# Kernel optimization log

Hardware: AMD Instinct MI355X
Metric: run time of the kernel (lower is better)

Reference implementation:

```python
import jax, jax.numpy as jnp
import numpy as np

NEG_SLOPE = 0.2

def edge_softmax(logits, dst, num_nodes):
    # logits: [E, H]; softmax over incoming edges of each dst node, per head
    m = jax.ops.segment_max(logits, dst, num_segments=num_nodes)  # [N, H]
    e = jnp.exp(logits - m[dst])
    s = jax.ops.segment_sum(e, dst, num_segments=num_nodes)  # [N, H]
    return e / s[dst]

def gat_layer(h, src, dst, W, al, ar, b, activation):
    # W: [F_in, H*D], al/ar: [H, D], b: [H, D]
    N = h.shape[0]
    H, D = al.shape
    feat = (h @ W).reshape(N, H, D)
    el = jnp.sum(feat * al, axis=-1)  # [N, H]
    er = jnp.sum(feat * ar, axis=-1)  # [N, H]
    e = jax.nn.leaky_relu(el[src] + er[dst], NEG_SLOPE)  # [E, H]
    a = edge_softmax(e, dst, N)  # [E, H]
    msg = feat[src] * a[:, :, None]  # [E, H, D]
    rst = jax.ops.segment_sum(msg, dst, num_segments=N) + b[None]  # [N, H, D]
    if activation:
        rst = jax.nn.relu(rst)
    return rst

def setup_inputs() -> dict:
    key = jax.random.key(0)
    ks = jax.random.split(key, 16)
    N, E = 50000, 800000
    IN, HID, OUT, H = 128, 64, 64, 4
    s = 0.1
    return {
        "features": jax.random.normal(ks[0], (N, IN), jnp.float32),
        "src": jax.random.randint(ks[1], (E,), 0, N),
        "dst": jax.random.randint(ks[2], (E,), 0, N),
        "W1": jax.random.normal(ks[3], (IN, H * HID), jnp.float32) * s,
        "al1": jax.random.normal(ks[4], (H, HID), jnp.float32) * s,
        "ar1": jax.random.normal(ks[5], (H, HID), jnp.float32) * s,
        "b1": jnp.zeros((H, HID), jnp.float32),
        "W2": jax.random.normal(ks[6], (H * HID, H * HID), jnp.float32) * s,
        "al2": jax.random.normal(ks[7], (H, HID), jnp.float32) * s,
        "ar2": jax.random.normal(ks[8], (H, HID), jnp.float32) * s,
        "b2": jnp.zeros((H, HID), jnp.float32),
        "W3": jax.random.normal(ks[9], (H * HID, OUT), jnp.float32) * s,
        "al3": jax.random.normal(ks[10], (1, OUT), jnp.float32) * s,
        "ar3": jax.random.normal(ks[11], (1, OUT), jnp.float32) * s,
        "b3": jnp.zeros((1, OUT), jnp.float32),
    }

def reference(features, src, dst, W1, al1, ar1, b1, W2, al2, ar2, b2, W3, al3, ar3, b3):
    N = features.shape[0]
    h = gat_layer(features, src, dst, W1, al1, ar1, b1, activation=True)   # [N, 4, 64]
    h = h.reshape(N, -1)                                                    # [N, 256]
    h = gat_layer(h, src, dst, W2, al2, ar2, b2, activation=True)          # [N, 4, 64]
    h = h.reshape(N, -1)                                                    # [N, 256]
    h = gat_layer(h, src, dst, W3, al3, ar3, b3, activation=False)         # [N, 1, 64]
    return h.mean(axis=1)                                                   # [N, 64]
```

## Files before the change

kernel.cpp:

```cpp
#include <hip/hip_runtime.h>
#include <hip/hip_bf16.h>

#define LEAKY 0.2f
#define LOG2E 1.44269504f

typedef __attribute__((ext_vector_type(8))) short short8;
typedef __attribute__((ext_vector_type(4))) float f32x4;

__device__ inline unsigned short f2b(float f) {
    unsigned u = __float_as_uint(f);
    u += 0x7FFFu + ((u >> 16) & 1u);
    return (unsigned short)(u >> 16);
}
__device__ inline float b2f(unsigned short s) {
    return __uint_as_float(((unsigned)s) << 16);
}
__device__ inline float fexp2(float x) { return __builtin_amdgcn_exp2f(x); }

#define NEB 8192



__global__ __launch_bounds__(256)
void k_prep(const float* __restrict__ features, unsigned short* __restrict__ fconv,
            int n4,
            const float* __restrict__ W1, const float* __restrict__ W2,
            const float* __restrict__ W3, unsigned short* __restrict__ Wt1,
            unsigned short* __restrict__ Wt2, unsigned short* __restrict__ Wt3,
            const int* __restrict__ dst, int* __restrict__ hist, int nbb,
            int E, int N) {
    __shared__ int lc[256];
    const int tid = threadIdx.x;
    if (blockIdx.x < nbb) {
        lc[tid] = 0;
        __syncthreads();
        const int b0 = blockIdx.x * NEB;
        const int cnt = min(NEB, E - b0);
        for (int j = 0; j < NEB / 256; ++j) {
            int idx = j * 256 + tid;
            if (idx < cnt) {
                int dn = dst[b0 + idx];
                if ((unsigned)dn < (unsigned)N) atomicAdd(&lc[dn >> 8], 1);
            }
        }
        __syncthreads();
        hist[blockIdx.x * 256 + tid] = lc[tid];
        return;
    }
    int idx = (blockIdx.x - nbb) * 256 + tid;
    if (idx < n4) {
        float4 v = *(const float4*)(features + idx * 4);
        ushort4 o;
        o.x = f2b(v.x); o.y = f2b(v.y); o.z = f2b(v.z); o.w = f2b(v.w);
        *(ushort4*)(fconv + idx * 4) = o;
        return;
    }
    int j = idx - n4;
    if (j < 32768) {
        int m = j >> 7, k = j & 127;
        Wt1[j] = f2b(W1[(size_t)k * 256 + m]);
        return;
    }
    if (j < 98304) {
        int jj = j - 32768;
        int m = jj >> 8, ks = jj & 255;
        int kt = (ks & 192) | ((ks & 3) << 4) | ((ks & 63) >> 2);
        Wt2[jj] = f2b(W2[(size_t)kt * 256 + m]);
        return;
    }
    if (j < 114688) {
        int jj = j - 98304;
        int m = jj >> 8, ks = jj & 255;
        int kt = (ks & 192) | ((ks & 3) << 4) | ((ks & 63) >> 2);
        Wt3[jj] = f2b(W3[(size_t)kt * 64 + m]);
    }
}


__global__ __launch_bounds__(256)
void k_bucket_scan(const int* __restrict__ hist, int nbb, int* __restrict__ bbase,
                   int* __restrict__ bcur, int* __restrict__ row_start_N, int B, int E) {
    __shared__ int ws[4];
    const int tid = threadIdx.x, lane = tid & 63, wave = tid >> 6;
    int v = 0;
    for (int blk = 0; blk < nbb; ++blk) v += hist[blk * 256 + tid];
    if (tid >= B) v = 0;
    int x = v;
    #pragma unroll
    for (int off = 1; off < 64; off <<= 1) {
        int t = __shfl_up(x, off, 64);
        if (lane >= off) x += t;
    }
    if (lane == 63) ws[wave] = x;
    __syncthreads();
    if (tid == 0) {
        int c = 0;
        #pragma unroll
        for (int wv = 0; wv < 4; ++wv) { int t = ws[wv]; ws[wv] = c; c += t; }
    }
    __syncthreads();
    int excl = x - v + ws[wave];
    if (tid < B) { bbase[tid] = excl; bcur[tid] = excl; }
    if (tid == 0) { bbase[B] = E; *row_start_N = E; }
}

__global__ __launch_bounds__(256)
void k_bin_scatter(const int* __restrict__ dst, int* __restrict__ bcur,
                   int* __restrict__ ebuf, int E, int N) {
    __shared__ int lc[256], lofs[256], lcur[256], gres[256];
    __shared__ int stage_e[NEB];
    __shared__ unsigned short stage_d[NEB];
    __shared__ int ws[4];
    const int tid = threadIdx.x, lane = tid & 63, wave = tid >> 6;
    const int b0 = blockIdx.x * NEB;
    const int cnt = min(NEB, E - b0);
    lc[tid] = 0;
    __syncthreads();

    int dreg[NEB / 256];
    #pragma unroll
    for (int j = 0; j < NEB / 256; ++j) {
        int idx = j * 256 + tid;
        dreg[j] = -1;
        if (idx < cnt) {
            int dn = dst[b0 + idx];
            if ((unsigned)dn < (unsigned)N) {
                dreg[j] = dn;
                atomicAdd(&lc[dn >> 8], 1);
            }
        }
    }
    __syncthreads();
    {
        int v = lc[tid];
        int x = v;
        #pragma unroll
        for (int off = 1; off < 64; off <<= 1) {
            int t = __shfl_up(x, off, 64);
            if (lane >= off) x += t;
        }
        if (lane == 63) ws[wave] = x;
        __syncthreads();
        if (tid == 0) {
            int c = 0;
            #pragma unroll
            for (int wv = 0; wv < 4; ++wv) { int t = ws[wv]; ws[wv] = c; c += t; }
        }
        __syncthreads();
        int excl = x - v + ws[wave];
        lofs[tid] = excl;
        lcur[tid] = excl;
    }
    __syncthreads();
    #pragma unroll
    for (int j = 0; j < NEB / 256; ++j) {
        int dn = dreg[j];
        if (dn >= 0) {
            int p = atomicAdd(&lcur[dn >> 8], 1);
            stage_e[p] = b0 + j * 256 + tid;
            stage_d[p] = (unsigned short)dn;
        }
    }
    __syncthreads();
    if (lc[tid] > 0) gres[tid] = atomicAdd(&bcur[tid], lc[tid]);
    __syncthreads();
    int total = lcur[255];
    for (int i = tid; i < total; i += 256) {
        int dn = stage_d[i];
        int k = dn >> 8;
        int dest = gres[k] + (i - lofs[k]);
        ebuf[dest] = ((dn & 255) << 24) | stage_e[i];
    }
}

__global__ __launch_bounds__(256)
void k_csr_build(const int* __restrict__ ebuf, const int* __restrict__ src,
                 const int* __restrict__ bbase, int* __restrict__ row_start,
                 int* __restrict__ src_sorted, int N) {
    __shared__ int lc[256], lcur[256];
    __shared__ int ws[4];
    const int tid = threadIdx.x, lane = tid & 63, wave = tid >> 6;
    const int k = blockIdx.x;
    const int base = k << 8;
    const int e0 = bbase[k];
    const int cnt = bbase[k + 1] - e0;
    lc[tid] = 0;
    __syncthreads();
    for (int i = tid; i < cnt; i += 256) {
        int rel = ((unsigned)ebuf[e0 + i]) >> 24;
        atomicAdd(&lc[rel], 1);
    }
    __syncthreads();
    {
        int v = lc[tid];
        int x = v;
        #pragma unroll
        for (int off = 1; off < 64; off <<= 1) {
            int t = __shfl_up(x, off, 64);
            if (lane >= off) x += t;
        }
        if (lane == 63) ws[wave] = x;
        __syncthreads();
        if (tid == 0) {
            int c = 0;
            #pragma unroll
            for (int wv = 0; wv < 4; ++wv) { int t = ws[wv]; ws[wv] = c; c += t; }
        }
        __syncthreads();
        int excl = x - v + ws[wave];
        lcur[tid] = excl;
        int n = base + tid;
        if (n < N) row_start[n] = e0 + excl;
    }
    __syncthreads();
    for (int i = tid; i < cnt; i += 256) {
        int val = ebuf[e0 + i];
        int rel = ((unsigned)val) >> 24;
        int e = val & 0xFFFFFF;
        int p = atomicAdd(&lcur[rel], 1);
        src_sorted[e0 + p] = src[e];
    }
}


__global__ __launch_bounds__(256)
void k_gemm_mfma(const unsigned short* __restrict__ A, const unsigned short* __restrict__ Wt,
                 unsigned short* __restrict__ Cb, const float* __restrict__ al,
                 const float* __restrict__ ar, float* __restrict__ el,
                 float* __restrict__ er, int N, int K, int M) {
    constexpr int STR = 40;
    __shared__ unsigned short As[128 * STR];
    __shared__ unsigned short Bs[128 * STR];
    const int tid  = threadIdx.x;
    const int wave = tid >> 6;
    const int lane = tid & 63;
    const int row0 = blockIdx.y * 128;
    const int col0 = blockIdx.x * 128;
    const int wr = (wave >> 1) * 64;
    const int wc = (wave & 1) * 64;
    const int m16 = lane & 15;
    const int q   = lane >> 4;

    const int s_row = tid >> 1;
    const int s_off = (tid & 1) * 16;

    f32x4 acc[4][4] = {};

    for (int k0 = 0; k0 < K; k0 += 32) {
        {
            int gr = row0 + s_row;
            short8 z = {};
            short8 v0 = z, v1 = z;
            if (gr < N) {
                const unsigned short* ap = A + (size_t)gr * K + k0 + s_off;
                v0 = *(const short8*)ap;
                v1 = *(const short8*)(ap + 8);
            }
            *(short8*)&As[s_row * STR + s_off]     = v0;
            *(short8*)&As[s_row * STR + s_off + 8] = v1;
        }
        {
            const unsigned short* sp = Wt + (size_t)(col0 + s_row) * K + k0 + s_off;
            *(short8*)&Bs[s_row * STR + s_off]     = *(const short8*)sp;
            *(short8*)&Bs[s_row * STR + s_off + 8] = *(const short8*)(sp + 8);
        }
        __syncthreads();

        short8 afr[4], bfr[4];
        #pragma unroll
        for (int rg = 0; rg < 4; ++rg)
            afr[rg] = *(const short8*)&As[(wr + rg * 16 + m16) * STR + q * 8];
        #pragma unroll
        for (int cg = 0; cg < 4; ++cg)
            bfr[cg] = *(const short8*)&Bs[(wc + cg * 16 + m16) * STR + q * 8];
        #pragma unroll
        for (int rg = 0; rg < 4; ++rg)
            #pragma unroll
            for (int cg = 0; cg < 4; ++cg)
                acc[rg][cg] = __builtin_amdgcn_mfma_f32_16x16x32_bf16(
                    afr[rg], bfr[cg], acc[rg][cg], 0, 0, 0);
        __syncthreads();
    }

    const int H = M >> 6;
    const int h = (col0 + wc) >> 6;
    float alv[4], arv[4];
    #pragma unroll
    for (int cg = 0; cg < 4; ++cg) {
        alv[cg] = al[h * 64 + cg * 16 + m16];
        arv[cg] = ar[h * 64 + cg * 16 + m16];
    }

    #pragma unroll
    for (int rg = 0; rg < 4; ++rg) {
        #pragma unroll
        for (int r = 0; r < 4; ++r) {
            int gr = row0 + wr + rg * 16 + q * 4 + r;
            float pl = 0.f, pr = 0.f;
            #pragma unroll
            for (int cg = 0; cg < 4; ++cg) {
                pl = fmaf(acc[rg][cg][r], alv[cg], pl);
                pr = fmaf(acc[rg][cg][r], arv[cg], pr);
            }
            #pragma unroll
            for (int off = 1; off < 16; off <<= 1) {
                pl += __shfl_xor(pl, off, 64);
                pr += __shfl_xor(pr, off, 64);
            }
            if (gr < N) {
                ushort4 o;
                o.x = f2b(acc[rg][0][r]); o.y = f2b(acc[rg][1][r]);
                o.z = f2b(acc[rg][2][r]); o.w = f2b(acc[rg][3][r]);
                *(ushort4*)(Cb + (size_t)gr * M + (col0 + wc) + m16 * 4) = o;
                if (m16 == 0) {
                    el[gr * H + h] = pl * LOG2E;
                    er[gr * H + h] = pr * LOG2E;
                }
            }
        }
    }
}


__global__ __launch_bounds__(256)
void k_gemm_mfma64(const unsigned short* __restrict__ A, const unsigned short* __restrict__ Wt,
                   unsigned short* __restrict__ Cb, const float* __restrict__ al,
                   const float* __restrict__ ar, float* __restrict__ el,
                   float* __restrict__ er, int N, int K) {
    constexpr int M = 64;
    constexpr int STR = 40;
    __shared__ unsigned short As[256 * STR];
    __shared__ unsigned short Bs[64 * STR];
    const int tid  = threadIdx.x;
    const int wave = tid >> 6;
    const int lane = tid & 63;
    const int row0 = blockIdx.x * 256;
    const int wr = wave * 64;
    const int m16 = lane & 15;
    const int q   = lane >> 4;

    const int s_row = tid >> 1;
    const int s_off = (tid & 1) * 16;
    const int b_row = tid >> 2;
    const int b_chk = (tid & 3) * 8;

    f32x4 acc[4][4] = {};

    for (int k0 = 0; k0 < K; k0 += 32) {
        #pragma unroll
        for (int p = 0; p < 2; ++p) {
            int r = s_row + p * 128;
            int gr = row0 + r;
            short8 z = {};
            short8 v0 = z, v1 = z;
            if (gr < N) {
                const unsigned short* ap = A + (size_t)gr * K + k0 + s_off;
                v0 = *(const short8*)ap;
                v1 = *(const short8*)(ap + 8);
            }
            *(short8*)&As[r * STR + s_off]     = v0;
            *(short8*)&As[r * STR + s_off + 8] = v1;
        }
        {
            const unsigned short* sp = Wt + (size_t)b_row * K + k0 + b_chk;
            *(short8*)&Bs[b_row * STR + b_chk] = *(const short8*)sp;
        }
        __syncthreads();

        short8 afr[4], bfr[4];
        #pragma unroll
        for (int rg = 0; rg < 4; ++rg)
            afr[rg] = *(const short8*)&As[(wr + rg * 16 + m16) * STR + q * 8];
        #pragma unroll
        for (int cg = 0; cg < 4; ++cg)
            bfr[cg] = *(const short8*)&Bs[(cg * 16 + m16) * STR + q * 8];
        #pragma unroll
        for (int rg = 0; rg < 4; ++rg)
            #pragma unroll
            for (int cg = 0; cg < 4; ++cg)
                acc[rg][cg] = __builtin_amdgcn_mfma_f32_16x16x32_bf16(
                    afr[rg], bfr[cg], acc[rg][cg], 0, 0, 0);
        __syncthreads();
    }

    float alv[4], arv[4];
    #pragma unroll
    for (int cg = 0; cg < 4; ++cg) {
        alv[cg] = al[cg * 16 + m16];
        arv[cg] = ar[cg * 16 + m16];
    }

    #pragma unroll
    for (int rg = 0; rg < 4; ++rg) {
        #pragma unroll
        for (int r = 0; r < 4; ++r) {
            int gr = row0 + wr + rg * 16 + q * 4 + r;
            float pl = 0.f, pr = 0.f;
            #pragma unroll
            for (int cg = 0; cg < 4; ++cg) {
                pl = fmaf(acc[rg][cg][r], alv[cg], pl);
                pr = fmaf(acc[rg][cg][r], arv[cg], pr);
            }
            #pragma unroll
            for (int off = 1; off < 16; off <<= 1) {
                pl += __shfl_xor(pl, off, 64);
                pr += __shfl_xor(pr, off, 64);
            }
            if (gr < N) {
                ushort4 o;
                o.x = f2b(acc[rg][0][r]); o.y = f2b(acc[rg][1][r]);
                o.z = f2b(acc[rg][2][r]); o.w = f2b(acc[rg][3][r]);
                *(ushort4*)(Cb + (size_t)gr * M + m16 * 4) = o;
                if (m16 == 0) {
                    el[gr] = pl * LOG2E;
                    er[gr] = pr * LOG2E;
                }
            }
        }
    }
}

template<int OUTBF, int HH>
__global__ __launch_bounds__(256)
void k_agg_f(const int* __restrict__ row_start, const int* __restrict__ src_sorted,
             const uint4* __restrict__ featp, const float* __restrict__ el,
             const float* __restrict__ er, const float* __restrict__ bias,
             void* __restrict__ outv, int N, int do_relu) {
    constexpr int M = HH * 64;
    constexpr int P = M >> 3;
    constexpr int G = 256 / P;
    const int grp = threadIdx.x / P;
    const int t = threadIdx.x - grp * P;
    const int n = blockIdx.x * G + grp;
    if (n >= N) return;
    const int d0 = t * 8;
    const int h = d0 >> 6;
    const float erv = er[n * HH + h];

    const int b0 = row_start[n], b1 = row_start[n + 1];

    float a[8] = {};
    float sum = 0.f;
    int i = b0;

    int ssP[8];
    if (i + 8 <= b1) {
        #pragma unroll
        for (int j = 0; j < 8; ++j) ssP[j] = src_sorted[i + j];
    }
    for (; i + 8 <= b1; i += 8) {
        int ss[8];
        #pragma unroll
        for (int j = 0; j < 8; ++j) ss[j] = ssP[j];
        if (i + 16 <= b1) {
            #pragma unroll
            for (int j = 0; j < 8; ++j) ssP[j] = src_sorted[i + 8 + j];
        }
        float wv[8]; uint4 pv[8];
        #pragma unroll
        for (int j = 0; j < 8; ++j) wv[j] = el[(unsigned)(ss[j] * HH + h)];
        #pragma unroll
        for (int j = 0; j < 8; ++j) pv[j] = featp[(unsigned)(ss[j] * P + t)];
        #pragma unroll
        for (int j = 0; j < 8; ++j) {
            float x = wv[j] + erv;
            x = fmaxf(x, LEAKY * x);
            float w = fexp2(x);
            wv[j] = w;
            sum += w;
        }
        #pragma unroll
        for (int j = 0; j < 8; ++j) {
            a[0] = fmaf(__uint_as_float(pv[j].x << 16),         wv[j], a[0]);
            a[1] = fmaf(__uint_as_float(pv[j].x & 0xFFFF0000u), wv[j], a[1]);
            a[2] = fmaf(__uint_as_float(pv[j].y << 16),         wv[j], a[2]);
            a[3] = fmaf(__uint_as_float(pv[j].y & 0xFFFF0000u), wv[j], a[3]);
            a[4] = fmaf(__uint_as_float(pv[j].z << 16),         wv[j], a[4]);
            a[5] = fmaf(__uint_as_float(pv[j].z & 0xFFFF0000u), wv[j], a[5]);
            a[6] = fmaf(__uint_as_float(pv[j].w << 16),         wv[j], a[6]);
            a[7] = fmaf(__uint_as_float(pv[j].w & 0xFFFF0000u), wv[j], a[7]);
        }
    }
    for (; i + 4 <= b1; i += 4) {
        int ss[4]; float wv[4]; uint4 pv[4];
        #pragma unroll
        for (int j = 0; j < 4; ++j) ss[j] = src_sorted[i + j];
        #pragma unroll
        for (int j = 0; j < 4; ++j) wv[j] = el[(unsigned)(ss[j] * HH + h)];
        #pragma unroll
        for (int j = 0; j < 4; ++j) pv[j] = featp[(unsigned)(ss[j] * P + t)];
        #pragma unroll
        for (int j = 0; j < 4; ++j) {
            float x = wv[j] + erv;
            x = fmaxf(x, LEAKY * x);
            float w = fexp2(x);
            wv[j] = w;
            sum += w;
        }
        #pragma unroll
        for (int j = 0; j < 4; ++j) {
            a[0] = fmaf(__uint_as_float(pv[j].x << 16),         wv[j], a[0]);
            a[1] = fmaf(__uint_as_float(pv[j].x & 0xFFFF0000u), wv[j], a[1]);
            a[2] = fmaf(__uint_as_float(pv[j].y << 16),         wv[j], a[2]);
            a[3] = fmaf(__uint_as_float(pv[j].y & 0xFFFF0000u), wv[j], a[3]);
            a[4] = fmaf(__uint_as_float(pv[j].z << 16),         wv[j], a[4]);
            a[5] = fmaf(__uint_as_float(pv[j].z & 0xFFFF0000u), wv[j], a[5]);
            a[6] = fmaf(__uint_as_float(pv[j].w << 16),         wv[j], a[6]);
            a[7] = fmaf(__uint_as_float(pv[j].w & 0xFFFF0000u), wv[j], a[7]);
        }
    }
    for (; i < b1; ++i) {
        int ss = src_sorted[i];
        float x = el[(unsigned)(ss * HH + h)] + erv;
        uint4 pv = featp[(unsigned)(ss * P + t)];
        x = fmaxf(x, LEAKY * x);
        float w = fexp2(x);
        sum += w;
        a[0] = fmaf(__uint_as_float(pv.x << 16),         w, a[0]);
        a[1] = fmaf(__uint_as_float(pv.x & 0xFFFF0000u), w, a[1]);
        a[2] = fmaf(__uint_as_float(pv.y << 16),         w, a[2]);
        a[3] = fmaf(__uint_as_float(pv.y & 0xFFFF0000u), w, a[3]);
        a[4] = fmaf(__uint_as_float(pv.z << 16),         w, a[4]);
        a[5] = fmaf(__uint_as_float(pv.z & 0xFFFF0000u), w, a[5]);
        a[6] = fmaf(__uint_as_float(pv.w << 16),         w, a[6]);
        a[7] = fmaf(__uint_as_float(pv.w & 0xFFFF0000u), w, a[7]);
    }

    float rs = 1.0f / fmaxf(sum, 1e-30f);
    const int c0 = (d0 & 63) >> 2;
    const float* bh = bias + h * 64 + c0;
    #pragma unroll
    for (int j = 0; j < 8; ++j)
        a[j] = fmaf(a[j], rs, bh[16 * (j & 3) + (j >> 2)]);
    if (do_relu) {
        #pragma unroll
        for (int j = 0; j < 8; ++j) a[j] = fmaxf(a[j], 0.f);
    }
    if (OUTBF) {
        uint4 o;
        o.x = (unsigned)f2b(a[0]) | ((unsigned)f2b(a[1]) << 16);
        o.y = (unsigned)f2b(a[2]) | ((unsigned)f2b(a[3]) << 16);
        o.z = (unsigned)f2b(a[4]) | ((unsigned)f2b(a[5]) << 16);
        o.w = (unsigned)f2b(a[6]) | ((unsigned)f2b(a[7]) << 16);
        *(uint4*)((unsigned short*)outv + (size_t)n * M + d0) = o;
    } else {
        float* op = (float*)outv + (size_t)n * M + h * 64 + c0;
        #pragma unroll
        for (int j = 0; j < 4; ++j)
            *(float2*)(op + 16 * j) = make_float2(a[j], a[j + 4]);
    }
}


static void run_layer(const unsigned short* A, int K, const unsigned short* Wt,
                      const float* al_, const float* ar_, const float* b_, int H,
                      unsigned short* featb, void* rstOut, bool outBf,
                      float* el, float* er,
                      const int* row_start, const int* src_sorted,
                      int N, int E, bool do_relu, hipStream_t stream) {
    const int M = H * 64;
    if (M % 128 == 0) {
        dim3 gg(M / 128, (N + 127) / 128);
        k_gemm_mfma<<<gg, 256, 0, stream>>>(A, Wt, featb, al_, ar_, el, er, N, K, M);
    } else {
        k_gemm_mfma64<<<(N + 255) / 256, 256, 0, stream>>>(A, Wt, featb, al_, ar_, el, er, N, K);
    }

    int G = 256 / (M / 8);
    int blocks = (N + G - 1) / G;
    if (H == 4) {
        if (outBf)
            k_agg_f<1, 4><<<blocks, 256, 0, stream>>>(row_start, src_sorted,
                                                      (const uint4*)featb, el, er,
                                                      b_, rstOut, N, do_relu ? 1 : 0);
        else
            k_agg_f<0, 4><<<blocks, 256, 0, stream>>>(row_start, src_sorted,
                                                      (const uint4*)featb, el, er,
                                                      b_, rstOut, N, do_relu ? 1 : 0);
    } else {
        if (outBf)
            k_agg_f<1, 1><<<blocks, 256, 0, stream>>>(row_start, src_sorted,
                                                      (const uint4*)featb, el, er,
                                                      b_, rstOut, N, do_relu ? 1 : 0);
        else
            k_agg_f<0, 1><<<blocks, 256, 0, stream>>>(row_start, src_sorted,
                                                      (const uint4*)featb, el, er,
                                                      b_, rstOut, N, do_relu ? 1 : 0);
    }
}

extern "C" void kernel_launch(void* const* d_in, const int* in_sizes, int n_in,
                              void* d_out, int out_size, void* d_ws, size_t ws_size,
                              hipStream_t stream) {
    const float* features = (const float*)d_in[0];
    const int*   src = (const int*)d_in[1];
    const int*   dst = (const int*)d_in[2];
    const float* W1  = (const float*)d_in[3];
    const float* al1 = (const float*)d_in[4];
    const float* ar1 = (const float*)d_in[5];
    const float* b1  = (const float*)d_in[6];
    const float* W2  = (const float*)d_in[7];
    const float* al2 = (const float*)d_in[8];
    const float* ar2 = (const float*)d_in[9];
    const float* b2  = (const float*)d_in[10];
    const float* W3  = (const float*)d_in[11];
    const float* al3 = (const float*)d_in[12];
    const float* ar3 = (const float*)d_in[13];
    const float* b3  = (const float*)d_in[14];

    const int N = in_sizes[0] / 128;
    const int E = in_sizes[1];
    const int B = (N + 255) >> 8;
    const int n4 = N * 128 / 4;
    const int nbb = (E + NEB - 1) / NEB;

    float* ws   = (float*)d_ws;
    float* el   = ws;
    float* er   = el + (size_t)N * 4;
    int* row_start  = (int*)(er + (size_t)N * 4);
    int* src_sorted = row_start + N + 1;
    int* ebuf       = src_sorted + E;
    int* bbase      = ebuf + E;
    int* bcur       = bbase + 257;
    int* hist       = bcur + 256;
    uintptr_t wp = (uintptr_t)(hist + (size_t)nbb * 256);
    wp = (wp + 15) & ~(uintptr_t)15;
    unsigned short* Wt1   = (unsigned short*)wp;
    unsigned short* Wt2   = Wt1 + 32768;
    unsigned short* Wt3   = Wt2 + 65536;
    unsigned short* fconv = Wt3 + 16384;
    unsigned short* featb = fconv + (size_t)N * 128;
    unsigned short* rstb  = featb + (size_t)N * 256;

    int prep_total = n4 + 114688;
    int prep_blocks = nbb + (prep_total + 255) / 256;
    k_prep<<<prep_blocks, 256, 0, stream>>>(features, fconv, n4,
                                            W1, W2, W3, Wt1, Wt2, Wt3,
                                            dst, hist, nbb, E, N);

    k_bucket_scan<<<1, 256, 0, stream>>>(hist, nbb, bbase, bcur, row_start + N, B, E);
    k_bin_scatter<<<nbb, 256, 0, stream>>>(dst, bcur, ebuf, E, N);
    k_csr_build<<<B, 256, 0, stream>>>(ebuf, src, bbase, row_start, src_sorted, N);

    run_layer(fconv, 128, Wt1, al1, ar1, b1, 4, featb, rstb, true,
              el, er, row_start, src_sorted, N, E, true, stream);
    run_layer(rstb, 256, Wt2, al2, ar2, b2, 4, featb, rstb, true,
              el, er, row_start, src_sorted, N, E, true, stream);
    run_layer(rstb, 256, Wt3, al3, ar3, b3, 1, featb, d_out, false,
              el, er, row_start, src_sorted, N, E, false, stream);
}
```

Baseline: 391.7 us.

## Fuse bucket scan into bin scatter, carry src in ebuf, use direct-to-LDS GEMM loads

Removes the single-block bucket-scan kernel. Each bin-scatter block now recomputes the global bucket prefix and its own offset from the per-block histograms, so no global atomics are needed. The src index is packed into ebuf in place of the edge id, which removes the random gather of src in the CSR build. The GEMM tile loads now use global_load_lds with an XOR-swizzled unpadded LDS layout instead of register-staged padded stores. This trades redundant histogram reads in every block for one fewer launch and less gather traffic, and it relies on node ids fitting in 24 bits and on a clamped row read replacing zero fill for out-of-range rows.

Result: no change. 385.0 us, median of 2 (-1.7%).

```diff
diff --git a/kernel.cpp b/kernel.cpp
--- a/kernel.cpp
+++ b/kernel.cpp
@@ -16,6 +16,13 @@
     return __uint_as_float(((unsigned)s) << 16);
 }
 __device__ inline float fexp2(float x) { return __builtin_amdgcn_exp2f(x); }
+
+__device__ inline void gload16(const void* g, void* l) {
+    __builtin_amdgcn_global_load_lds(
+        (const __attribute__((address_space(1))) unsigned int*)g,
+        (__attribute__((address_space(3))) unsigned int*)l,
+        16, 0, 0);
+}
 
 #define NEB 8192
 
@@ -78,38 +85,13 @@
 
 
 __global__ __launch_bounds__(256)
-void k_bucket_scan(const int* __restrict__ hist, int nbb, int* __restrict__ bbase,
-                   int* __restrict__ bcur, int* __restrict__ row_start_N, int B, int E) {
-    __shared__ int ws[4];
-    const int tid = threadIdx.x, lane = tid & 63, wave = tid >> 6;
-    int v = 0;
-    for (int blk = 0; blk < nbb; ++blk) v += hist[blk * 256 + tid];
-    if (tid >= B) v = 0;
-    int x = v;
-    #pragma unroll
-    for (int off = 1; off < 64; off <<= 1) {
-        int t = __shfl_up(x, off, 64);
-        if (lane >= off) x += t;
-    }
-    if (lane == 63) ws[wave] = x;
-    __syncthreads();
-    if (tid == 0) {
-        int c = 0;
-        #pragma unroll
-        for (int wv = 0; wv < 4; ++wv) { int t = ws[wv]; ws[wv] = c; c += t; }
-    }
-    __syncthreads();
-    int excl = x - v + ws[wave];
-    if (tid < B) { bbase[tid] = excl; bcur[tid] = excl; }
-    if (tid == 0) { bbase[B] = E; *row_start_N = E; }
-}
-
-__global__ __launch_bounds__(256)
-void k_bin_scatter(const int* __restrict__ dst, int* __restrict__ bcur,
-                   int* __restrict__ ebuf, int E, int N) {
+void k_bin_scatter(const int* __restrict__ dst, const int* __restrict__ src,
+                   const int* __restrict__ hist, int nbb,
+                   int* __restrict__ bbase, int* __restrict__ row_start,
+                   int* __restrict__ ebuf, int E, int N, int B) {
     __shared__ int lc[256], lofs[256], lcur[256], gres[256];
-    __shared__ int stage_e[NEB];
-    __shared__ unsigned short stage_d[NEB];
+    __shared__ int stage_v[NEB];
+    __shared__ unsigned short stage_b[NEB];
     __shared__ int ws[4];
     const int tid = threadIdx.x, lane = tid & 63, wave = tid >> 6;
     const int b0 = blockIdx.x * NEB;
@@ -117,7 +99,7 @@
     lc[tid] = 0;
     __syncthreads();
 
-    int dreg[NEB / 256];
+    int dreg[NEB / 256], sreg[NEB / 256];
     #pragma unroll
     for (int j = 0; j < NEB / 256; ++j) {
         int idx = j * 256 + tid;
@@ -126,8 +108,38 @@
             int dn = dst[b0 + idx];
             if ((unsigned)dn < (unsigned)N) {
                 dreg[j] = dn;
+                sreg[j] = src[b0 + idx];
                 atomicAdd(&lc[dn >> 8], 1);
             }
+        }
+    }
+
+    int pre = 0, tot = 0;
+    for (int b = 0; b < nbb; ++b) {
+        int hv = hist[b * 256 + tid];
+        tot += hv;
+        if (b < (int)blockIdx.x) pre += hv;
+    }
+    {
+        int x = tot;
+        #pragma unroll
+        for (int off = 1; off < 64; off <<= 1) {
+            int t = __shfl_up(x, off, 64);
+            if (lane >= off) x += t;
+        }
+        if (lane == 63) ws[wave] = x;
+        __syncthreads();
+        if (tid == 0) {
+            int c = 0;
+            #pragma unroll
+            for (int wv = 0; wv < 4; ++wv) { int t = ws[wv]; ws[wv] = c; c += t; }
+        }
+        __syncthreads();
+        int excl = x - tot + ws[wave];
+        gres[tid] = excl + pre;
+        if (blockIdx.x == 0) {
+            bbase[tid] = excl;
+            if (tid == 0) { bbase[256] = E; row_start[N] = E; }
         }
     }
     __syncthreads();
@@ -157,24 +169,21 @@
         int dn = dreg[j];
         if (dn >= 0) {
             int p = atomicAdd(&lcur[dn >> 8], 1);
-            stage_e[p] = b0 + j * 256 + tid;
-            stage_d[p] = (unsigned short)dn;
-        }
-    }
-    __syncthreads();
-    if (lc[tid] > 0) gres[tid] = atomicAdd(&bcur[tid], lc[tid]);
+            stage_v[p] = ((dn & 255) << 24) | sreg[j];
+            stage_b[p] = (unsigned short)(dn >> 8);
+        }
+    }
     __syncthreads();
     int total = lcur[255];
     for (int i = tid; i < total; i += 256) {
-        int dn = stage_d[i];
-        int k = dn >> 8;
-        int dest = gres[k] + (i - lofs[k]);
-        ebuf[dest] = ((dn & 255) << 24) | stage_e[i];
+        int k = stage_b[i];
+        int destp = gres[k] + (i - lofs[k]);
+        ebuf[destp] = stage_v[i];
     }
 }
 
 __global__ __launch_bounds__(256)
-void k_csr_build(const int* __restrict__ ebuf, const int* __restrict__ src,
+void k_csr_build(const int* __restrict__ ebuf,
                  const int* __restrict__ bbase, int* __restrict__ row_start,
                  int* __restrict__ src_sorted, int N) {
     __shared__ int lc[256], lcur[256];
@@ -216,9 +225,8 @@
     for (int i = tid; i < cnt; i += 256) {
         int val = ebuf[e0 + i];
         int rel = ((unsigned)val) >> 24;
-        int e = val & 0xFFFFFF;
         int p = atomicAdd(&lcur[rel], 1);
-        src_sorted[e0 + p] = src[e];
+        src_sorted[e0 + p] = val & 0xFFFFFF;
     }
 }
 
@@ -228,9 +236,8 @@
                  unsigned short* __restrict__ Cb, const float* __restrict__ al,
                  const float* __restrict__ ar, float* __restrict__ el,
                  float* __restrict__ er, int N, int K, int M) {
-    constexpr int STR = 40;
-    __shared__ unsigned short As[128 * STR];
-    __shared__ unsigned short Bs[128 * STR];
+    __shared__ unsigned short As[128 * 32];
+    __shared__ unsigned short Bs[128 * 32];
     const int tid  = threadIdx.x;
     const int wave = tid >> 6;
     const int lane = tid & 63;
@@ -241,38 +248,31 @@
     const int m16 = lane & 15;
     const int q   = lane >> 4;
 
-    const int s_row = tid >> 1;
-    const int s_off = (tid & 1) * 16;
+    const int c0   = wave * 2;
+    const int rA   = c0 * 16 + (lane >> 2);
+    const int sc   = (((lane & 3) ^ ((lane >> 3) & 3)) << 3);
+    const int qsw  = (q ^ ((m16 >> 1) & 3)) * 8;
 
     f32x4 acc[4][4] = {};
 
     for (int k0 = 0; k0 < K; k0 += 32) {
         {
-            int gr = row0 + s_row;
-            short8 z = {};
-            short8 v0 = z, v1 = z;
-            if (gr < N) {
-                const unsigned short* ap = A + (size_t)gr * K + k0 + s_off;
-                v0 = *(const short8*)ap;
-                v1 = *(const short8*)(ap + 8);
-            }
-            *(short8*)&As[s_row * STR + s_off]     = v0;
-            *(short8*)&As[s_row * STR + s_off + 8] = v1;
-        }
-        {
-            const unsigned short* sp = Wt + (size_t)(col0 + s_row) * K + k0 + s_off;
-            *(short8*)&Bs[s_row * STR + s_off]     = *(const short8*)sp;
-            *(short8*)&Bs[s_row * STR + s_off + 8] = *(const short8*)(sp + 8);
+            int g1 = row0 + rA;      if (g1 > N - 1) g1 = N - 1;
+            int g2 = row0 + rA + 16; if (g2 > N - 1) g2 = N - 1;
+            gload16(A + (size_t)g1 * K + k0 + sc, &As[c0 * 512]);
+            gload16(A + (size_t)g2 * K + k0 + sc, &As[c0 * 512 + 512]);
+            gload16(Wt + (size_t)(col0 + rA) * K + k0 + sc, &Bs[c0 * 512]);
+            gload16(Wt + (size_t)(col0 + rA + 16) * K + k0 + sc, &Bs[c0 * 512 + 512]);
         }
         __syncthreads();
 
         short8 afr[4], bfr[4];
         #pragma unroll
         for (int rg = 0; rg < 4; ++rg)
-            afr[rg] = *(const short8*)&As[(wr + rg * 16 + m16) * STR + q * 8];
+            afr[rg] = *(const short8*)&As[(wr + rg * 16 + m16) * 32 + qsw];
         #pragma unroll
         for (int cg = 0; cg < 4; ++cg)
-            bfr[cg] = *(const short8*)&Bs[(wc + cg * 16 + m16) * STR + q * 8];
+            bfr[cg] = *(const short8*)&Bs[(wc + cg * 16 + m16) * 32 + qsw];
         #pragma unroll
         for (int rg = 0; rg < 4; ++rg)
             #pragma unroll
@@ -621,8 +621,7 @@
     int* src_sorted = row_start + N + 1;
     int* ebuf       = src_sorted + E;
     int* bbase      = ebuf + E;
-    int* bcur       = bbase + 257;
-    int* hist       = bcur + 256;
+    int* hist       = bbase + 257;
     uintptr_t wp = (uintptr_t)(hist + (size_t)nbb * 256);
     wp = (wp + 15) & ~(uintptr_t)15;
     unsigned short* Wt1   = (unsigned short*)wp;
@@ -638,9 +637,9 @@
                                             W1, W2, W3, Wt1, Wt2, Wt3,
                                             dst, hist, nbb, E, N);
 
-    k_bucket_scan<<<1, 256, 0, stream>>>(hist, nbb, bbase, bcur, row_start + N, B, E);
-    k_bin_scatter<<<nbb, 256, 0, stream>>>(dst, bcur, ebuf, E, N);
-    k_csr_build<<<B, 256, 0, stream>>>(ebuf, src, bbase, row_start, src_sorted, N);
+    k_bin_scatter<<<nbb, 256, 0, stream>>>(dst, src, hist, nbb, bbase,
+                                           row_start, ebuf, E, N, B);
+    k_csr_build<<<B, 256, 0, stream>>>(ebuf, bbase, row_start, src_sorted, N);
 
     run_layer(fconv, 128, Wt1, al1, ar1, b1, 4, featb, rstb, true,
               el, er, row_start, src_sorted, N, E, true, stream);
```
